# Optimization experiments

Measured on AMD Instinct MI355X. Metric: run time of the kernel, lower is better.

The kernel has to match this reference:

```python
import jax, jax.numpy as jnp
import numpy as np

N = 100000          # nodes
E = 1600000         # directed edges
F_IN = 512          # num_features
H = 8               # heads
FH = 8              # per-head out channels
C = H * FH          # 64 hidden channels
HID = (2 * C) // 2  # 64, PyG JK lstm hidden size
NUM_CLASSES = 40
NEG_SLOPE = 0.2     # GATConv leaky relu slope


def setup_inputs() -> dict:
    key = jax.random.key(0)
    ks = jax.random.split(key, 24)
    s = 0.1
    inp = {
        "x": jax.random.normal(ks[0], (N, F_IN), jnp.float32),
        "edge_index": jax.random.randint(ks[1], (2, E), 0, N, jnp.int64)
        if jax.config.jax_enable_x64 else jax.random.randint(ks[1], (2, E), 0, N, jnp.int32),
        # GATConv 1
        "W1": jax.random.normal(ks[2], (F_IN, H * FH), jnp.float32) * s,
        "a1_src": jax.random.normal(ks[3], (H, FH), jnp.float32) * s,
        "a1_dst": jax.random.normal(ks[4], (H, FH), jnp.float32) * s,
        "b1": jnp.zeros((H * FH,), jnp.float32),
        # GATConv 2
        "W2": jax.random.normal(ks[5], (C, H * FH), jnp.float32) * s,
        "a2_src": jax.random.normal(ks[6], (H, FH), jnp.float32) * s,
        "a2_dst": jax.random.normal(ks[7], (H, FH), jnp.float32) * s,
        "b2": jnp.zeros((H * FH,), jnp.float32),
        # JK bidirectional LSTM (torch gate order i,f,g,o)
        "Wih_f": jax.random.normal(ks[8], (4 * HID, C), jnp.float32) * s,
        "Whh_f": jax.random.normal(ks[9], (4 * HID, HID), jnp.float32) * s,
        "bih_f": jnp.zeros((4 * HID,), jnp.float32),
        "bhh_f": jnp.zeros((4 * HID,), jnp.float32),
        "Wih_b": jax.random.normal(ks[10], (4 * HID, C), jnp.float32) * s,
        "Whh_b": jax.random.normal(ks[11], (4 * HID, HID), jnp.float32) * s,
        "bih_b": jnp.zeros((4 * HID,), jnp.float32),
        "bhh_b": jnp.zeros((4 * HID,), jnp.float32),
        # JK attention head
        "w_att": jax.random.normal(ks[12], (2 * HID,), jnp.float32) * s,
        "b_att": jnp.zeros((), jnp.float32),
        # output layer (bias=False)
        "W_out": jax.random.normal(ks[13], (NUM_CLASSES, C), jnp.float32) * s,
    }
    return inp


def gat_layer(x, src, dst, W, a_src, a_dst, b):
    n = x.shape[0]
    h = (x @ W).reshape(n, H, FH)                       # [N,H,FH]
    al_s = jnp.einsum('nhf,hf->nh', h, a_src)           # [N,H]
    al_d = jnp.einsum('nhf,hf->nh', h, a_dst)
    e = jax.nn.leaky_relu(al_s[src] + al_d[dst], NEG_SLOPE)  # [E',H]
    m = jax.ops.segment_max(e, dst, num_segments=n)     # segment softmax over dst
    ex = jnp.exp(e - m[dst])
    ssum = jax.ops.segment_sum(ex, dst, num_segments=n)
    alpha = ex / ssum[dst]                              # [E',H]
    out = jax.ops.segment_sum(h[src] * alpha[:, :, None], dst, num_segments=n)
    return out.reshape(n, H * FH) + b


def lstm_dir(xs, Wih, Whh, bih, bhh):
    # xs: [L, N, C] -> hs: [L, N, HID]
    n = xs.shape[1]

    def step(carry, xt):
        hprev, cprev = carry
        g = xt @ Wih.T + bih + hprev @ Whh.T + bhh
        i, f, gg, o = jnp.split(g, 4, axis=-1)
        c = jax.nn.sigmoid(f) * cprev + jax.nn.sigmoid(i) * jnp.tanh(gg)
        hh = jax.nn.sigmoid(o) * jnp.tanh(c)
        return (hh, c), hh

    init = (jnp.zeros((n, HID), xs.dtype), jnp.zeros((n, HID), xs.dtype))
    _, hs = jax.lax.scan(step, init, xs)
    return hs


def reference(x, edge_index, W1, a1_src, a1_dst, b1, W2, a2_src, a2_dst, b2,
              Wih_f, Whh_f, bih_f, bhh_f, Wih_b, Whh_b, bih_b, bhh_b,
              w_att, b_att, W_out):
    n = x.shape[0]
    loop = jnp.arange(n, dtype=edge_index.dtype)        # PyG add_self_loops
    src = jnp.concatenate([edge_index[0], loop])
    dst = jnp.concatenate([edge_index[1], loop])

    # eval mode: dropouts are identity
    x1 = jax.nn.elu(gat_layer(x, src, dst, W1, a1_src, a1_dst, b1))   # [N,64]
    x2 = gat_layer(x1, src, dst, W2, a2_src, a2_dst, b2)              # [N,64]

    xs = jnp.stack([x1, x2], axis=0)                    # [L=2, N, 64]
    h_f = lstm_dir(xs, Wih_f, Whh_f, bih_f, bhh_f)
    h_b = lstm_dir(xs[::-1], Wih_b, Whh_b, bih_b, bhh_b)[::-1]
    hcat = jnp.concatenate([h_f, h_b], axis=-1)         # [2, N, 128]

    att = jnp.einsum('lnk,k->ln', hcat, w_att) + b_att  # [2, N]
    alpha = jax.nn.softmax(att, axis=0)
    final = jnp.sum(xs * alpha[:, :, None], axis=0)     # [N, 64]

    return jax.nn.log_softmax(final @ W_out.T, axis=-1)
```

## Files before the change

### kernel.cpp

```cpp
#include <hip/hip_runtime.h>
#include <math.h>

#define F_IN 512
#define NCLS 40
#define BSH 7
#define BNODES (1 << BSH)
#define CH 16384

typedef __attribute__((ext_vector_type(8))) short bf16x8;
typedef __attribute__((ext_vector_type(4))) float f32x4;

__device__ __forceinline__ f32x4 mfma_bf16(bf16x8 a, bf16x8 b, f32x4 c){
  return __builtin_amdgcn_mfma_f32_16x16x32_bf16(a, b, c, 0, 0, 0);
}
__device__ __forceinline__ float fsigm(float x){ return 1.f/(1.f+__expf(-x)); }
__device__ __forceinline__ float ftanh(float x){ return 1.f - 2.f/(__expf(2.f*x)+1.f); }
__device__ __forceinline__ unsigned short f2bf(float f){
  unsigned u = __float_as_uint(f);
  return (unsigned short)((u + 0x7fffu + ((u>>16)&1u)) >> 16);
}
__device__ __forceinline__ float bf2f(unsigned short h){
  return __uint_as_float(((unsigned)h) << 16);
}

__global__ __launch_bounds__(256) void k_pcount(const int* __restrict__ ei, int e, int n,
                                                int nb, int* __restrict__ bhist){
  __shared__ int h[1024];
  int b = blockIdx.x, t = threadIdx.x;
  for (int i = t; i < nb; i += 256) h[i] = 0;
  __syncthreads();
  int tot = e + n;
  int base = b*CH;
  int lim = min(base + CH, tot);
  for (int i = base + t; i < lim; i += 256){
    int d = (i < e) ? ei[e + i] : (i - e);
    atomicAdd(&h[d >> BSH], 1);
  }
  __syncthreads();
  for (int i = t; i < nb; i += 256) bhist[(size_t)b*nb + i] = h[i];
}

__global__ __launch_bounds__(256) void k_pscan1(int* __restrict__ bhist, int nb, int B,
                                                int* __restrict__ bcnt){
  int i = blockIdx.x*256 + threadIdx.x;
  if (i >= nb) return;
  int run = 0;
  for (int b = 0; b < B; b++){
    int v = bhist[(size_t)b*nb + i];
    bhist[(size_t)b*nb + i] = run;
    run += v;
  }
  bcnt[i] = run;
}

__global__ __launch_bounds__(256) void k_pscan2(const int* __restrict__ bcnt, int nb, int tot,
                                                int* __restrict__ bbase,
                                                int* __restrict__ rowptr, int n){
  __shared__ int sb[256];
  __shared__ int carry;
  int t = threadIdx.x;
  if (t == 0) carry = 0;
  __syncthreads();
  for (int c0 = 0; c0 < nb; c0 += 256){
    int v = (c0 + t < nb) ? bcnt[c0 + t] : 0;
    sb[t] = v; __syncthreads();
    for (int off = 1; off < 256; off <<= 1){
      int u = (t >= off) ? sb[t-off] : 0; __syncthreads();
      sb[t] += u; __syncthreads();
    }
    if (c0 + t < nb) bbase[c0 + t] = carry + sb[t] - v;
    __syncthreads();
    if (t == 0) carry += sb[255];
    __syncthreads();
  }
  if (t == 0){ bbase[nb] = carry; rowptr[n] = tot; }
}

__global__ __launch_bounds__(256) void k_pscatter(const int* __restrict__ ei, int e, int n,
                                                  int nb, const int* __restrict__ bhist,
                                                  const int* __restrict__ bbase,
                                                  unsigned* __restrict__ bedges){
  __shared__ int cur[1024];
  int b = blockIdx.x, t = threadIdx.x;
  for (int i = t; i < nb; i += 256)
    cur[i] = bbase[i] + bhist[(size_t)b*nb + i];
  __syncthreads();
  int tot = e + n;
  int base = b*CH;
  int lim = min(base + CH, tot);
  for (int i = base + t; i < lim; i += 256){
    int s, d;
    if (i < e){ s = ei[i]; d = ei[e + i]; } else { s = i - e; d = s; }
    int pos = atomicAdd(&cur[d >> BSH], 1);
    bedges[pos] = (unsigned)s | ((unsigned)(d & (BNODES-1)) << 20);
  }
}

__global__ __launch_bounds__(256) void k_bbuild(const unsigned* __restrict__ bedges,
                                                const int* __restrict__ bbase,
                                                int* __restrict__ rowptr, int* __restrict__ col, int n){
  int b = blockIdx.x;
  int t = threadIdx.x;
  __shared__ int hist[BNODES];
  __shared__ int sc[BNODES];
  __shared__ int cur[BNODES];
  int beg = bbase[b], end = bbase[b+1];
  if (t < BNODES) hist[t] = 0;
  __syncthreads();
  for (int i = beg + t; i < end; i += 256)
    atomicAdd(&hist[bedges[i] >> 20], 1);
  __syncthreads();
  int v = (t < BNODES) ? hist[t] : 0;
  if (t < BNODES) sc[t] = v;
  __syncthreads();
  for (int off = 1; off < BNODES; off <<= 1){
    int u = (t >= off && t < BNODES) ? sc[t-off] : 0;
    __syncthreads();
    if (t < BNODES) sc[t] += u;
    __syncthreads();
  }
  if (t < BNODES){
    int excl = sc[t] - v;
    int node = (b << BSH) + t;
    if (node < n) rowptr[node] = beg + excl;
    cur[t] = excl;
  }
  __syncthreads();
  for (int i = beg + t; i < end; i += 256){
    unsigned pk = bedges[i];
    int pos = atomicAdd(&cur[pk >> 20], 1);
    col[beg + pos] = (int)(pk & 0xFFFFFu);
  }
}

__global__ __launch_bounds__(256) void k_prep(
    const float* __restrict__ W1, const float* __restrict__ W2,
    const float* __restrict__ Wihf, const float* __restrict__ Whhf,
    const float* __restrict__ Wihb, const float* __restrict__ Whhb,
    unsigned short* __restrict__ W1T, unsigned short* __restrict__ W2T,
    unsigned short* __restrict__ Wfx, unsigned short* __restrict__ Wfh,
    unsigned short* __restrict__ Wbx, unsigned short* __restrict__ Wbh)
{
  int i = blockIdx.x*256 + threadIdx.x;
  if (i < 32768){
    int k = i >> 6, c = i & 63;
    W1T[c*512 + k] = f2bf(W1[i]);
  } else if (i < 36864){
    int j = i - 32768; int k = j >> 6, c = j & 63;
    W2T[c*64 + k] = f2bf(W2[j]);
  } else if (i < 102400){
    int j = i - 36864;
    int which = j >> 14, o = j & 16383;
    const float* src = which==0 ? Wihf : which==1 ? Whhf : which==2 ? Wihb : Whhb;
    unsigned short* dst = which==0 ? Wfx : which==1 ? Wfh : which==2 ? Wbx : Wbh;
    dst[o] = f2bf(src[o]);
  }
}

template<int K, bool SRCF32>
__global__ __launch_bounds__(256) void k_mf_gemm(
    const float* __restrict__ Xf, const unsigned short* __restrict__ Xh,
    const unsigned short* __restrict__ WT,
    const float* __restrict__ as_, const float* __restrict__ ad_,
    unsigned short* __restrict__ Hb, unsigned short* __restrict__ alsb,
    float* __restrict__ ald, int n)
{
  int t = threadIdx.x;
  int w = t >> 6, l = t & 63;
  int c = l & 15, kg = l >> 4;
  int n0 = blockIdx.x*64 + w*16;
  int row = min(n0 + c, n-1);
  f32x4 acc[4];
  #pragma unroll
  for (int j = 0; j < 4; j++) acc[j] = (f32x4){0.f,0.f,0.f,0.f};

  #pragma unroll 4
  for (int kt = 0; kt < K/32; ++kt){
    int ko = kt*32 + kg*8;
    bf16x8 a;
    if (SRCF32){
      const float* xp = Xf + (size_t)row*K + ko;
      float4 u0 = *reinterpret_cast<const float4*>(xp);
      float4 u1 = *reinterpret_cast<const float4*>(xp + 4);
      a[0]=(short)f2bf(u0.x); a[1]=(short)f2bf(u0.y); a[2]=(short)f2bf(u0.z); a[3]=(short)f2bf(u0.w);
      a[4]=(short)f2bf(u1.x); a[5]=(short)f2bf(u1.y); a[6]=(short)f2bf(u1.z); a[7]=(short)f2bf(u1.w);
    } else {
      a = *reinterpret_cast<const bf16x8*>(Xh + (size_t)row*K + ko);
    }
    #pragma unroll
    for (int j = 0; j < 4; j++){
      bf16x8 b = *reinterpret_cast<const bf16x8*>(WT + (size_t)(j*16 + c)*K + ko);
      acc[j] = mfma_bf16(a, b, acc[j]);
    }
  }
  float asl[4], adl[4];
  #pragma unroll
  for (int j = 0; j < 4; j++){ asl[j] = as_[j*16 + c]; adl[j] = ad_[j*16 + c]; }
  #pragma unroll
  for (int j = 0; j < 4; j++){
    #pragma unroll
    for (int r = 0; r < 4; r++){
      int grow = n0 + kg*4 + r;
      float v = acc[j][r];
      if (grow < n) Hb[(size_t)grow*64 + j*16 + c] = f2bf(v);
      float sv = v*asl[j];
      float dv = v*adl[j];
      sv += __shfl_xor(sv, 1, 64); sv += __shfl_xor(sv, 2, 64); sv += __shfl_xor(sv, 4, 64);
      dv += __shfl_xor(dv, 1, 64); dv += __shfl_xor(dv, 2, 64); dv += __shfl_xor(dv, 4, 64);
      if ((c & 7) == 0 && grow < n){
        int head = j*2 + (c >> 3);
        alsb[(size_t)grow*8 + head] = f2bf(sv);
        ald [(size_t)grow*8 + head] = dv;
      }
    }
  }
}

template<bool DO_ELU>
__global__ __launch_bounds__(256) void k_agg(
    const int* __restrict__ rowptr, const int* __restrict__ col,
    const unsigned short* __restrict__ Hb, const unsigned short* __restrict__ alsb,
    const float* __restrict__ ald, const float* __restrict__ bias,
    unsigned short* __restrict__ outb, int n)
{
  int half = threadIdx.x >> 5;
  int ln = threadIdx.x & 31;
  int node = blockIdx.x*8 + half;
  if (node >= n) return;
  int hh = ln >> 2;
  float adv = ald[node*8 + hh];
  int beg = rowptr[node], end = rowptr[node+1];
  const unsigned short* Hp = Hb + ln*2;
  const unsigned short* ap = alsb + hh;

  float ssum = 0.f, acc0 = 0.f, acc1 = 0.f;
  int p = beg;
  int s0 = col[p];
  int s1 = (p+1 < end) ? col[p+1] : s0;
  int s2 = (p+2 < end) ? col[p+2] : s0;
  int s3 = (p+3 < end) ? col[p+3] : s0;
  float a0 = bf2f(ap[s0*8]), a1 = bf2f(ap[s1*8]);
  float a2 = bf2f(ap[s2*8]), a3 = bf2f(ap[s3*8]);
  unsigned h0 = *reinterpret_cast<const unsigned*>(Hp + (size_t)s0*64);
  unsigned h1 = *reinterpret_cast<const unsigned*>(Hp + (size_t)s1*64);
  unsigned h2 = *reinterpret_cast<const unsigned*>(Hp + (size_t)s2*64);
  unsigned h3 = *reinterpret_cast<const unsigned*>(Hp + (size_t)s3*64);

  while (p < end){
    int np = p + 4;
    float b0=a0, b1=a1, b2=a2, b3=a3;
    unsigned g0=h0, g1=h1, g2=h2, g3=h3;
    if (np < end){
      s0 = col[np];
      s1 = (np+1 < end) ? col[np+1] : s0;
      s2 = (np+2 < end) ? col[np+2] : s0;
      s3 = (np+3 < end) ? col[np+3] : s0;
      a0 = bf2f(ap[s0*8]); a1 = bf2f(ap[s1*8]);
      a2 = bf2f(ap[s2*8]); a3 = bf2f(ap[s3*8]);
      h0 = *reinterpret_cast<const unsigned*>(Hp + (size_t)s0*64);
      h1 = *reinterpret_cast<const unsigned*>(Hp + (size_t)s1*64);
      h2 = *reinterpret_cast<const unsigned*>(Hp + (size_t)s2*64);
      h3 = *reinterpret_cast<const unsigned*>(Hp + (size_t)s3*64);
    }
    float e0 = b0 + adv; e0 = (e0>0.f)?e0:0.2f*e0;
    float e1 = b1 + adv; e1 = (e1>0.f)?e1:0.2f*e1;
    float e2 = b2 + adv; e2 = (e2>0.f)?e2:0.2f*e2;
    float e3 = b3 + adv; e3 = (e3>0.f)?e3:0.2f*e3;
    float x0 = __expf(e0);
    float x1 = (p+1 < end) ? __expf(e1) : 0.f;
    float x2 = (p+2 < end) ? __expf(e2) : 0.f;
    float x3 = (p+3 < end) ? __expf(e3) : 0.f;
    ssum += (x0 + x1) + (x2 + x3);
    acc0 = fmaf(x0, bf2f((unsigned short)g0), acc0);
    acc1 = fmaf(x0, bf2f((unsigned short)(g0>>16)), acc1);
    acc0 = fmaf(x1, bf2f((unsigned short)g1), acc0);
    acc1 = fmaf(x1, bf2f((unsigned short)(g1>>16)), acc1);
    acc0 = fmaf(x2, bf2f((unsigned short)g2), acc0);
    acc1 = fmaf(x2, bf2f((unsigned short)(g2>>16)), acc1);
    acc0 = fmaf(x3, bf2f((unsigned short)g3), acc0);
    acc1 = fmaf(x3, bf2f((unsigned short)(g3>>16)), acc1);
    p = np;
  }
  float inv = 1.f/ssum;
  float o0 = acc0*inv + bias[ln*2];
  float o1 = acc1*inv + bias[ln*2+1];
  if (DO_ELU){
    o0 = (o0 > 0.f) ? o0 : (__expf(o0) - 1.f);
    o1 = (o1 > 0.f) ? o1 : (__expf(o1) - 1.f);
  }
  unsigned pk = (unsigned)f2bf(o0) | ((unsigned)f2bf(o1) << 16);
  *reinterpret_cast<unsigned*>(outb + (size_t)node*64 + ln*2) = pk;
}

__global__ __launch_bounds__(256) void k_lstm0(
    const unsigned short* __restrict__ X1b, const unsigned short* __restrict__ X2b,
    const unsigned short* __restrict__ Wfx, const unsigned short* __restrict__ Wbx,
    const float* __restrict__ bihf, const float* __restrict__ bhhf,
    const float* __restrict__ bihb, const float* __restrict__ bhhb,
    const float* __restrict__ watt,
    unsigned short* __restrict__ Hf0, unsigned short* __restrict__ Cf0,
    unsigned short* __restrict__ Hb0, unsigned short* __restrict__ Cb0,
    float* __restrict__ pf0, float* __restrict__ pb0, int n)
{
  int dir = blockIdx.y;
  const unsigned short* X = dir ? X2b : X1b;
  const unsigned short* W = dir ? Wbx : Wfx;
  const float* bi = dir ? bihb : bihf;
  const float* bh = dir ? bhhb : bhhf;
  const float* wa = watt + dir*64;
  unsigned short* Ho = dir ? Hb0 : Hf0;
  unsigned short* Co = dir ? Cb0 : Cf0;
  float* po = dir ? pb0 : pf0;

  int t = threadIdx.x;
  int w = t >> 6, l = t & 63;
  int c = l & 15, kg = l >> 4;
  int n0 = blockIdx.x*32;
  int r0 = min(n0 + c, n-1);
  int r1 = min(n0 + 16 + c, n-1);
  f32x4 acc[2][4];
  #pragma unroll
  for (int m = 0; m < 2; m++)
    #pragma unroll
    for (int g = 0; g < 4; g++) acc[m][g] = (f32x4){0.f,0.f,0.f,0.f};

  #pragma unroll
  for (int kt = 0; kt < 2; ++kt){
    int ko = kt*32 + kg*8;
    bf16x8 a0 = *reinterpret_cast<const bf16x8*>(X + (size_t)r0*64 + ko);
    bf16x8 a1 = *reinterpret_cast<const bf16x8*>(X + (size_t)r1*64 + ko);
    #pragma unroll
    for (int g = 0; g < 4; g++){
      bf16x8 b = *reinterpret_cast<const bf16x8*>(W + (size_t)(g*64 + w*16 + c)*64 + ko);
      acc[0][g] = mfma_bf16(a0, b, acc[0][g]);
      acc[1][g] = mfma_bf16(a1, b, acc[1][g]);
    }
  }
  int hid = w*16 + c;
  float bs0 = bi[hid]       + bh[hid];
  float bs2 = bi[hid + 128] + bh[hid + 128];
  float bs3 = bi[hid + 192] + bh[hid + 192];
  float wav = wa[hid];
  __shared__ float attp[4][32];
  #pragma unroll
  for (int m = 0; m < 2; m++){
    #pragma unroll
    for (int r = 0; r < 4; r++){
      int rl = m*16 + kg*4 + r;
      int grow = n0 + rl;
      float gi = acc[m][0][r] + bs0;
      float gg = acc[m][2][r] + bs2;
      float go = acc[m][3][r] + bs3;
      float cc = fsigm(gi)*ftanh(gg);
      float hh = fsigm(go)*ftanh(cc);
      if (grow < n){
        Ho[(size_t)grow*64 + hid] = f2bf(hh);
        Co[(size_t)grow*64 + hid] = f2bf(cc);
      }
      float s = hh*wav;
      s += __shfl_xor(s, 1, 16);
      s += __shfl_xor(s, 2, 16);
      s += __shfl_xor(s, 4, 16);
      s += __shfl_xor(s, 8, 16);
      if (c == 0) attp[w][rl] = s;
    }
  }
  __syncthreads();
  if (t < 32){
    int grow = n0 + t;
    if (grow < n) po[grow] = attp[0][t] + attp[1][t] + attp[2][t] + attp[3][t];
  }
}

__global__ __launch_bounds__(256) void k_lstm1(
    const unsigned short* __restrict__ X1b, const unsigned short* __restrict__ X2b,
    const unsigned short* __restrict__ Hf0, const unsigned short* __restrict__ Cf0,
    const unsigned short* __restrict__ Hb0, const unsigned short* __restrict__ Cb0,
    const unsigned short* __restrict__ Wfx, const unsigned short* __restrict__ Wfh,
    const unsigned short* __restrict__ Wbx, const unsigned short* __restrict__ Wbh,
    const float* __restrict__ bihf, const float* __restrict__ bhhf,
    const float* __restrict__ bihb, const float* __restrict__ bhhb,
    const float* __restrict__ watt,
    float* __restrict__ pf1, float* __restrict__ pb1, int n)
{
  int dir = blockIdx.y;
  const unsigned short* X  = dir ? X1b : X2b;
  const unsigned short* Hp = dir ? Hb0 : Hf0;
  const unsigned short* Cp = dir ? Cb0 : Cf0;
  const unsigned short* Wx = dir ? Wbx : Wfx;
  const unsigned short* Wh = dir ? Wbh : Wfh;
  const float* bi = dir ? bihb : bihf;
  const float* bh = dir ? bhhb : bhhf;
  const float* wa = watt + dir*64;
  float* po = dir ? pb1 : pf1;

  int t = threadIdx.x;
  int w = t >> 6, l = t & 63;
  int c = l & 15, kg = l >> 4;
  int n0 = blockIdx.x*32;
  int r0 = min(n0 + c, n-1);
  int r1 = min(n0 + 16 + c, n-1);
  f32x4 acc[2][4];
  #pragma unroll
  for (int m = 0; m < 2; m++)
    #pragma unroll
    for (int g = 0; g < 4; g++) acc[m][g] = (f32x4){0.f,0.f,0.f,0.f};

  #pragma unroll
  for (int kt = 0; kt < 4; ++kt){
    const unsigned short* A = (kt < 2) ? X : Hp;
    const unsigned short* Wp = (kt < 2) ? Wx : Wh;
    int ko = (kt & 1)*32 + kg*8;
    bf16x8 a0 = *reinterpret_cast<const bf16x8*>(A + (size_t)r0*64 + ko);
    bf16x8 a1 = *reinterpret_cast<const bf16x8*>(A + (size_t)r1*64 + ko);
    #pragma unroll
    for (int g = 0; g < 4; g++){
      bf16x8 b = *reinterpret_cast<const bf16x8*>(Wp + (size_t)(g*64 + w*16 + c)*64 + ko);
      acc[0][g] = mfma_bf16(a0, b, acc[0][g]);
      acc[1][g] = mfma_bf16(a1, b, acc[1][g]);
    }
  }
  int hid = w*16 + c;
  float bs0 = bi[hid]       + bh[hid];
  float bs1 = bi[hid + 64]  + bh[hid + 64];
  float bs2 = bi[hid + 128] + bh[hid + 128];
  float bs3 = bi[hid + 192] + bh[hid + 192];
  float wav = wa[hid];
  __shared__ float attp[4][32];
  #pragma unroll
  for (int m = 0; m < 2; m++){
    #pragma unroll
    for (int r = 0; r < 4; r++){
      int rl = m*16 + kg*4 + r;
      int grow = n0 + rl;
      int crow = min(grow, n-1);
      float gi = acc[m][0][r] + bs0;
      float gf = acc[m][1][r] + bs1;
      float gg = acc[m][2][r] + bs2;
      float go = acc[m][3][r] + bs3;
      float cp = bf2f(Cp[(size_t)crow*64 + hid]);
      float cc = fsigm(gf)*cp + fsigm(gi)*ftanh(gg);
      float hh = fsigm(go)*ftanh(cc);
      float s = hh*wav;
      s += __shfl_xor(s, 1, 16);
      s += __shfl_xor(s, 2, 16);
      s += __shfl_xor(s, 4, 16);
      s += __shfl_xor(s, 8, 16);
      if (c == 0) attp[w][rl] = s;
    }
  }
  __syncthreads();
  if (t < 32){
    int grow = n0 + t;
    if (grow < n) po[grow] = attp[0][t] + attp[1][t] + attp[2][t] + attp[3][t];
  }
}

__global__ __launch_bounds__(256) void k_final(
    const unsigned short* __restrict__ x1b, const unsigned short* __restrict__ x2b,
    const float* __restrict__ pf0, const float* __restrict__ pf1,
    const float* __restrict__ pb0, const float* __restrict__ pb1,
    const float* __restrict__ Wout, float* __restrict__ out, int n)
{
  __shared__ __align__(16) float ws[NCLS][68];
  __shared__ __align__(16) float fs[32][68];
  int t = threadIdx.x;
  for (int i = t; i < NCLS*64; i += 256)
    ws[i>>6][i&63] = Wout[i];

  int n0 = blockIdx.x*32;
  int nd = t >> 3, q8 = t & 7;
  int g = n0 + nd;
  int eb = q8*8;
  if (g < n){
    float att0 = pf0[g] + pb1[g];
    float att1 = pf1[g] + pb0[g];
    float a0 = 1.f/(1.f + __expf(att1 - att0));
    float a1 = 1.f - a0;
    uint4 p1 = *reinterpret_cast<const uint4*>(x1b + (size_t)g*64 + eb);
    uint4 p2 = *reinterpret_cast<const uint4*>(x2b + (size_t)g*64 + eb);
    const unsigned* u1 = (const unsigned*)&p1;
    const unsigned* u2 = (const unsigned*)&p2;
    #pragma unroll
    for (int q = 0; q < 4; q++){
      float v1l = bf2f((unsigned short)u1[q]), v1h = bf2f((unsigned short)(u1[q]>>16));
      float v2l = bf2f((unsigned short)u2[q]), v2h = bf2f((unsigned short)(u2[q]>>16));
      fs[nd][eb + q*2 + 0] = a0*v1l + a1*v2l;
      fs[nd][eb + q*2 + 1] = a0*v1h + a1*v2h;
    }
  } else {
    #pragma unroll
    for (int q = 0; q < 8; q++) fs[nd][eb+q] = 0.f;
  }
  __syncthreads();

  float lg[5] = {0.f,0.f,0.f,0.f,0.f};
  #pragma unroll
  for (int k4 = 0; k4 < 16; k4++){
    float4 f = *reinterpret_cast<const float4*>(&fs[nd][k4*4]);
    #pragma unroll
    for (int q = 0; q < 5; q++){
      int cc = q8 + 8*q;
      float4 wv = *reinterpret_cast<const float4*>(&ws[cc][k4*4]);
      lg[q] = fmaf(f.x, wv.x, lg[q]);
      lg[q] = fmaf(f.y, wv.y, lg[q]);
      lg[q] = fmaf(f.z, wv.z, lg[q]);
      lg[q] = fmaf(f.w, wv.w, lg[q]);
    }
  }
  float mx = lg[0];
  #pragma unroll
  for (int q = 1; q < 5; q++) mx = fmaxf(mx, lg[q]);
  #pragma unroll
  for (int mk = 1; mk < 8; mk <<= 1) mx = fmaxf(mx, __shfl_xor(mx, mk, 64));
  float se = 0.f;
  #pragma unroll
  for (int q = 0; q < 5; q++) se += __expf(lg[q] - mx);
  #pragma unroll
  for (int mk = 1; mk < 8; mk <<= 1) se += __shfl_xor(se, mk, 64);
  float lse = __logf(se);
  if (g < n){
    #pragma unroll
    for (int q = 0; q < 5; q++)
      out[(size_t)g*NCLS + q8 + 8*q] = lg[q] - mx - lse;
  }
}

extern "C" void kernel_launch(void* const* d_in, const int* in_sizes, int n_in,
                              void* d_out, int out_size, void* d_ws, size_t ws_size,
                              hipStream_t stream)
{
  const float* x    = (const float*)d_in[0];
  const int*   ei   = (const int*)d_in[1];
  const float* W1   = (const float*)d_in[2];
  const float* a1s  = (const float*)d_in[3];
  const float* a1d  = (const float*)d_in[4];
  const float* b1   = (const float*)d_in[5];
  const float* W2   = (const float*)d_in[6];
  const float* a2s  = (const float*)d_in[7];
  const float* a2d  = (const float*)d_in[8];
  const float* b2   = (const float*)d_in[9];
  const float* Wih_f= (const float*)d_in[10];
  const float* Whh_f= (const float*)d_in[11];
  const float* bih_f= (const float*)d_in[12];
  const float* bhh_f= (const float*)d_in[13];
  const float* Wih_b= (const float*)d_in[14];
  const float* Whh_b= (const float*)d_in[15];
  const float* bih_b= (const float*)d_in[16];
  const float* bhh_b= (const float*)d_in[17];
  const float* watt = (const float*)d_in[18];
  const float* Wout = (const float*)d_in[20];
  float* out = (float*)d_out;

  int n = in_sizes[0] / F_IN;
  int e = in_sizes[1] / 2;
  int nb = (n + BNODES - 1) >> BSH;
  int B  = (e + n + CH - 1) / CH;

  char* p = (char*)d_ws;
  auto alloc = [&](size_t b)->char*{ char* r = p; p += (b + 255) & ~(size_t)255; return r; };
  int* rowptr = (int*)alloc((size_t)(n+1)*4);
  int* colidx = (int*)alloc((size_t)(e+n)*4);
  unsigned* bedges = (unsigned*)alloc((size_t)(e+n)*4);
  int* bhist  = (int*)alloc((size_t)B*nb*4);
  int* bcnt   = (int*)alloc((size_t)(nb+1)*4);
  int* bbase  = (int*)alloc((size_t)(nb+1)*4);
  unsigned short* hbuf = (unsigned short*)alloc((size_t)n*64*2);
  unsigned short* alsb = (unsigned short*)alloc((size_t)n*8*2);
  float* ald  = (float*)alloc((size_t)n*8*4);
  unsigned short* x1b = (unsigned short*)alloc((size_t)n*64*2);
  unsigned short* x2b = (unsigned short*)alloc((size_t)n*64*2);
  unsigned short* hf0 = (unsigned short*)alloc((size_t)n*64*2);
  unsigned short* cf0 = (unsigned short*)alloc((size_t)n*64*2);
  unsigned short* hb0 = (unsigned short*)alloc((size_t)n*64*2);
  unsigned short* cb0 = (unsigned short*)alloc((size_t)n*64*2);
  float* pf0 = (float*)alloc((size_t)n*4);
  float* pf1 = (float*)alloc((size_t)n*4);
  float* pb0 = (float*)alloc((size_t)n*4);
  float* pb1 = (float*)alloc((size_t)n*4);
  unsigned short* W1T = (unsigned short*)alloc((size_t)64*512*2);
  unsigned short* W2T = (unsigned short*)alloc((size_t)64*64*2);
  unsigned short* Wfx = (unsigned short*)alloc((size_t)256*64*2);
  unsigned short* Wfh = (unsigned short*)alloc((size_t)256*64*2);
  unsigned short* Wbx = (unsigned short*)alloc((size_t)256*64*2);
  unsigned short* Wbh = (unsigned short*)alloc((size_t)256*64*2);

  k_pcount<<<B, 256, 0, stream>>>(ei, e, n, nb, bhist);
  k_pscan1<<<(nb+255)/256, 256, 0, stream>>>(bhist, nb, B, bcnt);
  k_pscan2<<<1, 256, 0, stream>>>(bcnt, nb, e+n, bbase, rowptr, n);
  k_pscatter<<<B, 256, 0, stream>>>(ei, e, n, nb, bhist, bbase, bedges);
  k_bbuild<<<nb, 256, 0, stream>>>(bedges, bbase, rowptr, colidx, n);

  k_prep<<<400, 256, 0, stream>>>(W1, W2, Wih_f, Whh_f, Wih_b, Whh_b,
                                  W1T, W2T, Wfx, Wfh, Wbx, Wbh);

  int gblk = (n + 63)/64;
  k_mf_gemm<512,true ><<<gblk, 256, 0, stream>>>(x, nullptr, W1T, a1s, a1d, hbuf, alsb, ald, n);
  k_agg<true ><<<(n+7)/8, 256, 0, stream>>>(rowptr, colidx, hbuf, alsb, ald, b1, x1b, n);
  k_mf_gemm<64,false ><<<gblk, 256, 0, stream>>>(nullptr, x1b, W2T, a2s, a2d, hbuf, alsb, ald, n);
  k_agg<false><<<(n+7)/8, 256, 0, stream>>>(rowptr, colidx, hbuf, alsb, ald, b2, x2b, n);

  dim3 lgrid((n + 31)/32, 2);
  k_lstm0<<<lgrid, 256, 0, stream>>>(x1b, x2b, Wfx, Wbx, bih_f, bhh_f, bih_b, bhh_b,
                                     watt, hf0, cf0, hb0, cb0, pf0, pb0, n);
  k_lstm1<<<lgrid, 256, 0, stream>>>(x1b, x2b, hf0, cf0, hb0, cb0,
                                     Wfx, Wfh, Wbx, Wbh, bih_f, bhh_f, bih_b, bhh_b,
                                     watt, pf1, pb1, n);

  k_final<<<(n+3)/4, 256, 0, stream>>>(x1b, x2b, pf0, pf1, pb0, pb1, Wout, out, n);
}
```

Baseline: 562.5 us.

## Fuse the two LSTM steps into one kernel and widen aggregation per lane

```diff
diff --git a/kernel.cpp b/kernel.cpp
--- a/kernel.cpp
+++ b/kernel.cpp
@@ -223,17 +223,17 @@
     const float* __restrict__ ald, const float* __restrict__ bias,
     unsigned short* __restrict__ outb, int n)
 {
-  int half = threadIdx.x >> 5;
-  int ln = threadIdx.x & 31;
-  int node = blockIdx.x*8 + half;
+  int grp = threadIdx.x >> 4;
+  int ln  = threadIdx.x & 15;
+  int node = blockIdx.x*16 + grp;
   if (node >= n) return;
-  int hh = ln >> 2;
+  int hh = ln >> 1;
   float adv = ald[node*8 + hh];
   int beg = rowptr[node], end = rowptr[node+1];
-  const unsigned short* Hp = Hb + ln*2;
+  const unsigned short* Hp = Hb + ln*4;
   const unsigned short* ap = alsb + hh;
 
-  float ssum = 0.f, acc0 = 0.f, acc1 = 0.f;
+  float ssum = 0.f, acc0 = 0.f, acc1 = 0.f, acc2 = 0.f, acc3 = 0.f;
   int p = beg;
   int s0 = col[p];
   int s1 = (p+1 < end) ? col[p+1] : s0;
@@ -241,15 +241,15 @@
   int s3 = (p+3 < end) ? col[p+3] : s0;
   float a0 = bf2f(ap[s0*8]), a1 = bf2f(ap[s1*8]);
   float a2 = bf2f(ap[s2*8]), a3 = bf2f(ap[s3*8]);
-  unsigned h0 = *reinterpret_cast<const unsigned*>(Hp + (size_t)s0*64);
-  unsigned h1 = *reinterpret_cast<const unsigned*>(Hp + (size_t)s1*64);
-  unsigned h2 = *reinterpret_cast<const unsigned*>(Hp + (size_t)s2*64);
-  unsigned h3 = *reinterpret_cast<const unsigned*>(Hp + (size_t)s3*64);
+  ushort4 h0 = *reinterpret_cast<const ushort4*>(Hp + (size_t)s0*64);
+  ushort4 h1 = *reinterpret_cast<const ushort4*>(Hp + (size_t)s1*64);
+  ushort4 h2 = *reinterpret_cast<const ushort4*>(Hp + (size_t)s2*64);
+  ushort4 h3 = *reinterpret_cast<const ushort4*>(Hp + (size_t)s3*64);
 
   while (p < end){
     int np = p + 4;
     float b0=a0, b1=a1, b2=a2, b3=a3;
-    unsigned g0=h0, g1=h1, g2=h2, g3=h3;
+    ushort4 g0=h0, g1=h1, g2=h2, g3=h3;
     if (np < end){
       s0 = col[np];
       s1 = (np+1 < end) ? col[np+1] : s0;
@@ -257,10 +257,10 @@
       s3 = (np+3 < end) ? col[np+3] : s0;
       a0 = bf2f(ap[s0*8]); a1 = bf2f(ap[s1*8]);
       a2 = bf2f(ap[s2*8]); a3 = bf2f(ap[s3*8]);
-      h0 = *reinterpret_cast<const unsigned*>(Hp + (size_t)s0*64);
-      h1 = *reinterpret_cast<const unsigned*>(Hp + (size_t)s1*64);
-      h2 = *reinterpret_cast<const unsigned*>(Hp + (size_t)s2*64);
-      h3 = *reinterpret_cast<const unsigned*>(Hp + (size_t)s3*64);
+      h0 = *reinterpret_cast<const ushort4*>(Hp + (size_t)s0*64);
+      h1 = *reinterpret_cast<const ushort4*>(Hp + (size_t)s1*64);
+      h2 = *reinterpret_cast<const ushort4*>(Hp + (size_t)s2*64);
+      h3 = *reinterpret_cast<const ushort4*>(Hp + (size_t)s3*64);
     }
     float e0 = b0 + adv; e0 = (e0>0.f)?e0:0.2f*e0;
     float e1 = b1 + adv; e1 = (e1>0.f)?e1:0.2f*e1;
@@ -271,46 +271,55 @@
     float x2 = (p+2 < end) ? __expf(e2) : 0.f;
     float x3 = (p+3 < end) ? __expf(e3) : 0.f;
     ssum += (x0 + x1) + (x2 + x3);
-    acc0 = fmaf(x0, bf2f((unsigned short)g0), acc0);
-    acc1 = fmaf(x0, bf2f((unsigned short)(g0>>16)), acc1);
-    acc0 = fmaf(x1, bf2f((unsigned short)g1), acc0);
-    acc1 = fmaf(x1, bf2f((unsigned short)(g1>>16)), acc1);
-    acc0 = fmaf(x2, bf2f((unsigned short)g2), acc0);
-    acc1 = fmaf(x2, bf2f((unsigned short)(g2>>16)), acc1);
-    acc0 = fmaf(x3, bf2f((unsigned short)g3), acc0);
-    acc1 = fmaf(x3, bf2f((unsigned short)(g3>>16)), acc1);
+    acc0 = fmaf(x0, bf2f(g0.x), acc0); acc1 = fmaf(x0, bf2f(g0.y), acc1);
+    acc2 = fmaf(x0, bf2f(g0.z), acc2); acc3 = fmaf(x0, bf2f(g0.w), acc3);
+    acc0 = fmaf(x1, bf2f(g1.x), acc0); acc1 = fmaf(x1, bf2f(g1.y), acc1);
+    acc2 = fmaf(x1, bf2f(g1.z), acc2); acc3 = fmaf(x1, bf2f(g1.w), acc3);
+    acc0 = fmaf(x2, bf2f(g2.x), acc0); acc1 = fmaf(x2, bf2f(g2.y), acc1);
+    acc2 = fmaf(x2, bf2f(g2.z), acc2); acc3 = fmaf(x2, bf2f(g2.w), acc3);
+    acc0 = fmaf(x3, bf2f(g3.x), acc0); acc1 = fmaf(x3, bf2f(g3.y), acc1);
+    acc2 = fmaf(x3, bf2f(g3.z), acc2); acc3 = fmaf(x3, bf2f(g3.w), acc3);
     p = np;
   }
   float inv = 1.f/ssum;
-  float o0 = acc0*inv + bias[ln*2];
-  float o1 = acc1*inv + bias[ln*2+1];
+  float o0 = acc0*inv + bias[ln*4+0];
+  float o1 = acc1*inv + bias[ln*4+1];
+  float o2 = acc2*inv + bias[ln*4+2];
+  float o3 = acc3*inv + bias[ln*4+3];
   if (DO_ELU){
     o0 = (o0 > 0.f) ? o0 : (__expf(o0) - 1.f);
     o1 = (o1 > 0.f) ? o1 : (__expf(o1) - 1.f);
-  }
-  unsigned pk = (unsigned)f2bf(o0) | ((unsigned)f2bf(o1) << 16);
-  *reinterpret_cast<unsigned*>(outb + (size_t)node*64 + ln*2) = pk;
-}
-
-__global__ __launch_bounds__(256) void k_lstm0(
+    o2 = (o2 > 0.f) ? o2 : (__expf(o2) - 1.f);
+    o3 = (o3 > 0.f) ? o3 : (__expf(o3) - 1.f);
+  }
+  ushort4 pk;
+  pk.x = f2bf(o0); pk.y = f2bf(o1); pk.z = f2bf(o2); pk.w = f2bf(o3);
+  *reinterpret_cast<ushort4*>(outb + (size_t)node*64 + ln*4) = pk;
+}
+
+__global__ __launch_bounds__(256) void k_lstm(
     const unsigned short* __restrict__ X1b, const unsigned short* __restrict__ X2b,
-    const unsigned short* __restrict__ Wfx, const unsigned short* __restrict__ Wbx,
+    const unsigned short* __restrict__ Wfx, const unsigned short* __restrict__ Wfh,
+    const unsigned short* __restrict__ Wbx, const unsigned short* __restrict__ Wbh,
     const float* __restrict__ bihf, const float* __restrict__ bhhf,
     const float* __restrict__ bihb, const float* __restrict__ bhhb,
     const float* __restrict__ watt,
-    unsigned short* __restrict__ Hf0, unsigned short* __restrict__ Cf0,
-    unsigned short* __restrict__ Hb0, unsigned short* __restrict__ Cb0,
-    float* __restrict__ pf0, float* __restrict__ pb0, int n)
+    float* __restrict__ pf0, float* __restrict__ pf1,
+    float* __restrict__ pb0, float* __restrict__ pb1, int n)
 {
   int dir = blockIdx.y;
-  const unsigned short* X = dir ? X2b : X1b;
-  const unsigned short* W = dir ? Wbx : Wfx;
+  const unsigned short* X0 = dir ? X2b : X1b;
+  const unsigned short* X1 = dir ? X1b : X2b;
+  const unsigned short* Wx = dir ? Wbx : Wfx;
+  const unsigned short* Wh = dir ? Wbh : Wfh;
   const float* bi = dir ? bihb : bihf;
   const float* bh = dir ? bhhb : bhhf;
   const float* wa = watt + dir*64;
-  unsigned short* Ho = dir ? Hb0 : Hf0;
-  unsigned short* Co = dir ? Cb0 : Cf0;
-  float* po = dir ? pb0 : pf0;
+  float* po0 = dir ? pb0 : pf0;
+  float* po1 = dir ? pb1 : pf1;
+
+  __shared__ unsigned short hls[32][72];
+  __shared__ float attp[2][4][32];
 
   int t = threadIdx.x;
   int w = t >> 6, l = t & 63;
@@ -318,141 +327,106 @@
   int n0 = blockIdx.x*32;
   int r0 = min(n0 + c, n-1);
   int r1 = min(n0 + 16 + c, n-1);
-  f32x4 acc[2][4];
-  #pragma unroll
-  for (int m = 0; m < 2; m++)
-    #pragma unroll
-    for (int g = 0; g < 4; g++) acc[m][g] = (f32x4){0.f,0.f,0.f,0.f};
-
-  #pragma unroll
-  for (int kt = 0; kt < 2; ++kt){
-    int ko = kt*32 + kg*8;
-    bf16x8 a0 = *reinterpret_cast<const bf16x8*>(X + (size_t)r0*64 + ko);
-    bf16x8 a1 = *reinterpret_cast<const bf16x8*>(X + (size_t)r1*64 + ko);
-    #pragma unroll
-    for (int g = 0; g < 4; g++){
-      bf16x8 b = *reinterpret_cast<const bf16x8*>(W + (size_t)(g*64 + w*16 + c)*64 + ko);
-      acc[0][g] = mfma_bf16(a0, b, acc[0][g]);
-      acc[1][g] = mfma_bf16(a1, b, acc[1][g]);
-    }
-  }
-  int hid = w*16 + c;
-  float bs0 = bi[hid]       + bh[hid];
-  float bs2 = bi[hid + 128] + bh[hid + 128];
-  float bs3 = bi[hid + 192] + bh[hid + 192];
-  float wav = wa[hid];
-  __shared__ float attp[4][32];
-  #pragma unroll
-  for (int m = 0; m < 2; m++){
-    #pragma unroll
-    for (int r = 0; r < 4; r++){
-      int rl = m*16 + kg*4 + r;
-      int grow = n0 + rl;
-      float gi = acc[m][0][r] + bs0;
-      float gg = acc[m][2][r] + bs2;
-      float go = acc[m][3][r] + bs3;
-      float cc = fsigm(gi)*ftanh(gg);
-      float hh = fsigm(go)*ftanh(cc);
-      if (grow < n){
-        Ho[(size_t)grow*64 + hid] = f2bf(hh);
-        Co[(size_t)grow*64 + hid] = f2bf(cc);
-      }
-      float s = hh*wav;
-      s += __shfl_xor(s, 1, 16);
-      s += __shfl_xor(s, 2, 16);
-      s += __shfl_xor(s, 4, 16);
-      s += __shfl_xor(s, 8, 16);
-      if (c == 0) attp[w][rl] = s;
-    }
-  }
-  __syncthreads();
-  if (t < 32){
-    int grow = n0 + t;
-    if (grow < n) po[grow] = attp[0][t] + attp[1][t] + attp[2][t] + attp[3][t];
-  }
-}
-
-__global__ __launch_bounds__(256) void k_lstm1(
-    const unsigned short* __restrict__ X1b, const unsigned short* __restrict__ X2b,
-    const unsigned short* __restrict__ Hf0, const unsigned short* __restrict__ Cf0,
-    const unsigned short* __restrict__ Hb0, const unsigned short* __restrict__ Cb0,
-    const unsigned short* __restrict__ Wfx, const unsigned short* __restrict__ Wfh,
-    const unsigned short* __restrict__ Wbx, const unsigned short* __restrict__ Wbh,
-    const float* __restrict__ bihf, const float* __restrict__ bhhf,
-    const float* __restrict__ bihb, const float* __restrict__ bhhb,
-    const float* __restrict__ watt,
-    float* __restrict__ pf1, float* __restrict__ pb1, int n)
-{
-  int dir = blockIdx.y;
-  const unsigned short* X  = dir ? X1b : X2b;
-  const unsigned short* Hp = dir ? Hb0 : Hf0;
-  const unsigned short* Cp = dir ? Cb0 : Cf0;
-  const unsigned short* Wx = dir ? Wbx : Wfx;
-  const unsigned short* Wh = dir ? Wbh : Wfh;
-  const float* bi = dir ? bihb : bihf;
-  const float* bh = dir ? bhhb : bhhf;
-  const float* wa = watt + dir*64;
-  float* po = dir ? pb1 : pf1;
-
-  int t = threadIdx.x;
-  int w = t >> 6, l = t & 63;
-  int c = l & 15, kg = l >> 4;
-  int n0 = blockIdx.x*32;
-  int r0 = min(n0 + c, n-1);
-  int r1 = min(n0 + 16 + c, n-1);
-  f32x4 acc[2][4];
-  #pragma unroll
-  for (int m = 0; m < 2; m++)
-    #pragma unroll
-    for (int g = 0; g < 4; g++) acc[m][g] = (f32x4){0.f,0.f,0.f,0.f};
-
-  #pragma unroll
-  for (int kt = 0; kt < 4; ++kt){
-    const unsigned short* A = (kt < 2) ? X : Hp;
-    const unsigned short* Wp = (kt < 2) ? Wx : Wh;
-    int ko = (kt & 1)*32 + kg*8;
-    bf16x8 a0 = *reinterpret_cast<const bf16x8*>(A + (size_t)r0*64 + ko);
-    bf16x8 a1 = *reinterpret_cast<const bf16x8*>(A + (size_t)r1*64 + ko);
-    #pragma unroll
-    for (int g = 0; g < 4; g++){
-      bf16x8 b = *reinterpret_cast<const bf16x8*>(Wp + (size_t)(g*64 + w*16 + c)*64 + ko);
-      acc[0][g] = mfma_bf16(a0, b, acc[0][g]);
-      acc[1][g] = mfma_bf16(a1, b, acc[1][g]);
-    }
-  }
+
   int hid = w*16 + c;
   float bs0 = bi[hid]       + bh[hid];
   float bs1 = bi[hid + 64]  + bh[hid + 64];
   float bs2 = bi[hid + 128] + bh[hid + 128];
   float bs3 = bi[hid + 192] + bh[hid + 192];
   float wav = wa[hid];
-  __shared__ float attp[4][32];
+
+  f32x4 acc[2][4];
+  #pragma unroll
+  for (int m = 0; m < 2; m++)
+    #pragma unroll
+    for (int g = 0; g < 4; g++) acc[m][g] = (f32x4){0.f,0.f,0.f,0.f};
+
+  #pragma unroll
+  for (int kt = 0; kt < 2; ++kt){
+    int ko = kt*32 + kg*8;
+    bf16x8 a0 = *reinterpret_cast<const bf16x8*>(X0 + (size_t)r0*64 + ko);
+    bf16x8 a1 = *reinterpret_cast<const bf16x8*>(X0 + (size_t)r1*64 + ko);
+    #pragma unroll
+    for (int g = 0; g < 4; g++){
+      bf16x8 b = *reinterpret_cast<const bf16x8*>(Wx + (size_t)(g*64 + hid)*64 + ko);
+      acc[0][g] = mfma_bf16(a0, b, acc[0][g]);
+      acc[1][g] = mfma_bf16(a1, b, acc[1][g]);
+    }
+  }
+  float creg[2][4];
   #pragma unroll
   for (int m = 0; m < 2; m++){
     #pragma unroll
     for (int r = 0; r < 4; r++){
       int rl = m*16 + kg*4 + r;
-      int grow = n0 + rl;
-      int crow = min(grow, n-1);
+      float gi = acc[m][0][r] + bs0;
+      float gg = acc[m][2][r] + bs2;
+      float go = acc[m][3][r] + bs3;
+      float cc = fsigm(gi)*ftanh(gg);
+      float hh = fsigm(go)*ftanh(cc);
+      creg[m][r] = cc;
+      hls[rl][hid] = f2bf(hh);
+      float s = hh*wav;
+      s += __shfl_xor(s, 1, 16);
+      s += __shfl_xor(s, 2, 16);
+      s += __shfl_xor(s, 4, 16);
+      s += __shfl_xor(s, 8, 16);
+      if (c == 0) attp[0][w][rl] = s;
+    }
+  }
+  __syncthreads();
+
+  #pragma unroll
+  for (int m = 0; m < 2; m++)
+    #pragma unroll
+    for (int g = 0; g < 4; g++) acc[m][g] = (f32x4){0.f,0.f,0.f,0.f};
+
+  #pragma unroll
+  for (int kt = 0; kt < 4; ++kt){
+    int ko = (kt & 1)*32 + kg*8;
+    bf16x8 a0, a1;
+    if (kt < 2){
+      a0 = *reinterpret_cast<const bf16x8*>(X1 + (size_t)r0*64 + ko);
+      a1 = *reinterpret_cast<const bf16x8*>(X1 + (size_t)r1*64 + ko);
+    } else {
+      a0 = *reinterpret_cast<const bf16x8*>(&hls[c][ko]);
+      a1 = *reinterpret_cast<const bf16x8*>(&hls[16 + c][ko]);
+    }
+    const unsigned short* Wp = (kt < 2) ? Wx : Wh;
+    #pragma unroll
+    for (int g = 0; g < 4; g++){
+      bf16x8 b = *reinterpret_cast<const bf16x8*>(Wp + (size_t)(g*64 + hid)*64 + ko);
+      acc[0][g] = mfma_bf16(a0, b, acc[0][g]);
+      acc[1][g] = mfma_bf16(a1, b, acc[1][g]);
+    }
+  }
+  #pragma unroll
+  for (int m = 0; m < 2; m++){
+    #pragma unroll
+    for (int r = 0; r < 4; r++){
+      int rl = m*16 + kg*4 + r;
       float gi = acc[m][0][r] + bs0;
       float gf = acc[m][1][r] + bs1;
       float gg = acc[m][2][r] + bs2;
       float go = acc[m][3][r] + bs3;
-      float cp = bf2f(Cp[(size_t)crow*64 + hid]);
-      float cc = fsigm(gf)*cp + fsigm(gi)*ftanh(gg);
+      float cc = fsigm(gf)*creg[m][r] + fsigm(gi)*ftanh(gg);
       float hh = fsigm(go)*ftanh(cc);
       float s = hh*wav;
       s += __shfl_xor(s, 1, 16);
       s += __shfl_xor(s, 2, 16);
       s += __shfl_xor(s, 4, 16);
       s += __shfl_xor(s, 8, 16);
-      if (c == 0) attp[w][rl] = s;
+      if (c == 0) attp[1][w][rl] = s;
     }
   }
   __syncthreads();
   if (t < 32){
     int grow = n0 + t;
-    if (grow < n) po[grow] = attp[0][t] + attp[1][t] + attp[2][t] + attp[3][t];
+    if (grow < n) po0[grow] = attp[0][0][t] + attp[0][1][t] + attp[0][2][t] + attp[0][3][t];
+  } else if (t < 64){
+    int rr = t - 32;
+    int grow = n0 + rr;
+    if (grow < n) po1[grow] = attp[1][0][rr] + attp[1][1][rr] + attp[1][2][rr] + attp[1][3][rr];
   }
 }
 
@@ -570,10 +544,6 @@
   float* ald  = (float*)alloc((size_t)n*8*4);
   unsigned short* x1b = (unsigned short*)alloc((size_t)n*64*2);
   unsigned short* x2b = (unsigned short*)alloc((size_t)n*64*2);
-  unsigned short* hf0 = (unsigned short*)alloc((size_t)n*64*2);
-  unsigned short* cf0 = (unsigned short*)alloc((size_t)n*64*2);
-  unsigned short* hb0 = (unsigned short*)alloc((size_t)n*64*2);
-  unsigned short* cb0 = (unsigned short*)alloc((size_t)n*64*2);
   float* pf0 = (float*)alloc((size_t)n*4);
   float* pf1 = (float*)alloc((size_t)n*4);
   float* pb0 = (float*)alloc((size_t)n*4);
@@ -596,16 +566,14 @@
 
   int gblk = (n + 63)/64;
   k_mf_gemm<512,true ><<<gblk, 256, 0, stream>>>(x, nullptr, W1T, a1s, a1d, hbuf, alsb, ald, n);
-  k_agg<true ><<<(n+7)/8, 256, 0, stream>>>(rowptr, colidx, hbuf, alsb, ald, b1, x1b, n);
+  k_agg<true ><<<(n+15)/16, 256, 0, stream>>>(rowptr, colidx, hbuf, alsb, ald, b1, x1b, n);
   k_mf_gemm<64,false ><<<gblk, 256, 0, stream>>>(nullptr, x1b, W2T, a2s, a2d, hbuf, alsb, ald, n);
-  k_agg<false><<<(n+7)/8, 256, 0, stream>>>(rowptr, colidx, hbuf, alsb, ald, b2, x2b, n);
+  k_agg<false><<<(n+15)/16, 256, 0, stream>>>(rowptr, colidx, hbuf, alsb, ald, b2, x2b, n);
 
   dim3 lgrid((n + 31)/32, 2);
-  k_lstm0<<<lgrid, 256, 0, stream>>>(x1b, x2b, Wfx, Wbx, bih_f, bhh_f, bih_b, bhh_b,
-                                     watt, hf0, cf0, hb0, cb0, pf0, pb0, n);
-  k_lstm1<<<lgrid, 256, 0, stream>>>(x1b, x2b, hf0, cf0, hb0, cb0,
-                                     Wfx, Wfh, Wbx, Wbh, bih_f, bhh_f, bih_b, bhh_b,
-                                     watt, pf1, pb1, n);
+  k_lstm<<<lgrid, 256, 0, stream>>>(x1b, x2b, Wfx, Wfh, Wbx, Wbh,
+                                    bih_f, bhh_f, bih_b, bhh_b,
+                                    watt, pf0, pf1, pb0, pb1, n);
 
   k_final<<<(n+3)/4, 256, 0, stream>>>(x1b, x2b, pf0, pf1, pb0, pb1, Wout, out, n);
 }
```

Result: faster. 497.9 us (-11.5%).
